# Optimization experiments

Measured on AMD Instinct MI355X. Metric: run time of the kernel, lower is better.

The kernel has to match this reference:

```python
import jax, jax.numpy as jnp
import numpy as np
from jax import lax

STRIDE = (1, 1)  # module init arg; stride slicing of the spectrum


def next_pow2(k: int) -> int:
    return 1 << (int(k) - 1).bit_length()


def setup_inputs() -> dict:
    key = jax.random.key(0)
    k1, k2, k3 = jax.random.split(key, 3)
    B, H, W, C, F = 16, 128, 128, 16, 32
    image = jax.random.normal(k1, (B, H, W, C), dtype=jnp.float32)
    # kernel shape per module: (2*H/stride_h, W/stride_w + 1, features, C)
    kh, kw = 2 * H // STRIDE[0], W // STRIDE[1] + 1
    kernel_real = jax.random.normal(k2, (kh, kw, F, C), dtype=jnp.float32)
    kernel_imag = jax.random.normal(k3, (kh, kw, F, C), dtype=jnp.float32)
    bias = jnp.zeros((F,), dtype=jnp.float32)
    return {"image": image, "kernel_real": kernel_real,
            "kernel_imag": kernel_imag, "bias": bias}


def reference(image, kernel_real, kernel_imag, bias):
    kernel = kernel_real + 1j * kernel_imag  # complex64 [kh, kw, F, C]
    B, H, W, C = image.shape
    padded = (2 * H - 1, 2 * W - 1)                       # "full" conv extent
    fast = (next_pow2(padded[0]), next_pow2(padded[1]))    # FFT-friendly pad
    fast_strided = (next_pow2(kernel.shape[0]), next_pow2(kernel.shape[1]))
    # rfft2 over spatial axes -> [B, fast_h, fast_w//2+1, C]
    F_img = jnp.fft.rfft2(image, s=fast, axes=(1, 2))
    F_img = F_img[:, ::STRIDE[0], ::STRIDE[1]]
    # channel contraction in Fourier space (vmap+sum in original == einsum)
    out_f = jnp.einsum('bhwc,hwfc->bhwf', F_img, kernel)
    # back to real space: [B, fast_strided_h, fast_strided_w, F]
    conv = jnp.fft.irfft2(out_f, s=fast_strided, axes=(1, 2))
    conv = conv + bias
    # crop to full-conv extent, then center-crop to "same" shape
    conv = conv[:, :padded[0], :padded[1], :]
    sh = (padded[0] - H) // 2
    sw = (padded[1] - W) // 2
    return lax.slice(conv, (0, sh, sw, 0),
                     (B, sh + H, sw + W, conv.shape[-1]))
```

## Files before the change

### kernel.cpp

```cpp
#include <hip/hip_runtime.h>
#include <math.h>


constexpr int Bn = 16, Cc = 16, Ff = 32, Hh = 128, Ww = 128, Nn = 256, WH = 129;

#define DEVINL __device__ __forceinline__
DEVINL float2 f2(float a, float b) { return make_float2(a, b); }
DEVINL float2 cmul(float2 a, float2 b) { return f2(a.x * b.x - a.y * b.y, a.x * b.y + a.y * b.x); }

DEVINL unsigned short f2bf(float f) { unsigned u = __float_as_uint(f); return (unsigned short)((u + 0x8000u) >> 16); }
DEVINL float bf2f(unsigned short h) { return __uint_as_float(((unsigned)h) << 16); }
DEVINL unsigned packbf(float a, float b) { return (unsigned)f2bf(a) | ((unsigned)f2bf(b) << 16); }
DEVINL ushort2 pk2(float2 z) { return make_ushort2(f2bf(z.x), f2bf(z.y)); }
DEVINL float2 up2(ushort2 u) { return f2(bf2f(u.x), bf2f(u.y)); }

typedef __attribute__((ext_vector_type(8))) short short8;
typedef __attribute__((ext_vector_type(4))) float f32x4;

DEVINL int IDX(int r, int e) { return r * 256 + ((e + r) & 255); }

template<int SGN>
DEVINL void fft16r(float2 v[16]) {
  float2 t;
#define SW(a,b) { t = v[a]; v[a] = v[b]; v[b] = t; }
  SW(1, 8) SW(2, 4) SW(3, 12) SW(5, 10) SW(7, 14) SW(11, 13)
#undef SW
  const float C1 = 0.92387953251128674f, C2 = 0.70710678118654752f, C3 = 0.38268343236508977f;
  const float Ct[8] = {1.f, C1, C2, C3, 0.f, -C3, -C2, -C1};
  const float St[8] = {0.f, C3, C2, C1, 1.f, C1, C2, C3};
#pragma unroll
  for (int len = 2; len <= 16; len <<= 1) {
    const int half = len >> 1, ts = 16 / len;
#pragma unroll
    for (int i = 0; i < 16; i += len) {
#pragma unroll
      for (int j = 0; j < half; ++j) {
        const float wr = Ct[j * ts];
        const float wi = (SGN > 0) ? St[j * ts] : -St[j * ts];
        float2 b = v[i + j + half];
        float2 tt = f2(wr * b.x - wi * b.y, wr * b.y + wi * b.x);
        float2 a = v[i + j];
        v[i + j]        = f2(a.x + tt.x, a.y + tt.y);
        v[i + j + half] = f2(a.x - tt.x, a.y - tt.y);
      }
    }
  }
}

template<int SGN>
DEVINL void twiddle16(float2 v[16], int t) {
  const float unit = (SGN > 0) ? 0.024543692606170259f : -0.024543692606170259f;
  float sb, cb;
  __sincosf(unit * (float)t, &sb, &cb);
  float2 W[16];
  W[1] = f2(cb, sb);
#pragma unroll
  for (int k = 2; k < 16; ++k) W[k] = cmul(W[k >> 1], W[k - (k >> 1)]);
#pragma unroll
  for (int k = 1; k < 16; ++k) v[k] = cmul(v[k], W[k]);
}

template<int SGN>
DEVINL void fft256_mid(float2 v[16], float2* __restrict__ lds, int r, int t) {
  fft16r<SGN>(v);
  twiddle16<SGN>(v, t);
#pragma unroll
  for (int k = 0; k < 16; ++k) lds[IDX(r, t * 16 + ((k + t) & 15))] = v[k];
#pragma unroll
  for (int n2 = 0; n2 < 16; ++n2) v[n2] = lds[IDX(r, n2 * 16 + ((t + n2) & 15))];
  fft16r<SGN>(v);
}

__global__ __launch_bounds__(256) void k1_rowfft(const float* __restrict__ img, ushort2* __restrict__ R) {
  __shared__ float2 lds[16 * 256];
  const int tid = threadIdx.x, r = tid >> 4, t = tid & 15;
  const int y = blockIdx.x, b = blockIdx.y;
  const float* ip = img + ((size_t)(b * Hh + y) * Ww) * Cc;
  for (int i = tid; i < Ww * Cc; i += 256) { int x = i >> 4, c = i & 15; lds[IDX(c, x)] = f2(ip[i], 0.f); }
  __syncthreads();
  float2 v[16];
#pragma unroll
  for (int j = 0; j < 8; ++j) v[j] = lds[IDX(r, t + 16 * j)];
#pragma unroll
  for (int j = 8; j < 16; ++j) v[j] = f2(0.f, 0.f);
  fft256_mid<-1>(v, lds, r, t);
#pragma unroll
  for (int k = 0; k < 8; ++k) lds[IDX(r, t + 16 * k)] = v[k];
  if (t == 0) lds[IDX(r, 128)] = v[8];
  __syncthreads();
  ushort2* rp = R + (size_t)b * WH * Hh * Cc + (size_t)y * Cc;
  for (int i = tid; i < WH * Cc; i += 256) {
    int w = i >> 4, c = i & 15;
    rp[(size_t)w * Hh * Cc + c] = pk2(lds[IDX(c, w)]);
  }
}

__global__ __launch_bounds__(256) void k2_colfft(const ushort2* __restrict__ R, ushort2* __restrict__ Fimg) {
  __shared__ float2 lds[16 * 256];
  const int tid = threadIdx.x, r = tid >> 4, t = tid & 15;
  const int w = blockIdx.x, b = blockIdx.y;
  const ushort2* rp = R + ((size_t)(b * WH + w) * Hh) * Cc;
  for (int i = tid; i < Hh * Cc; i += 256) { int y = i >> 4, c = i & 15; lds[IDX(c, y)] = up2(rp[i]); }
  __syncthreads();
  float2 v[16];
#pragma unroll
  for (int j = 0; j < 8; ++j) v[j] = lds[IDX(r, t + 16 * j)];
#pragma unroll
  for (int j = 8; j < 16; ++j) v[j] = f2(0.f, 0.f);
  fft256_mid<-1>(v, lds, r, t);
#pragma unroll
  for (int k2 = 0; k2 < 16; ++k2) lds[IDX(r, t + 16 * k2)] = v[k2];
  __syncthreads();
  ushort2* fp = Fimg + (size_t)w * 256 + b * 16;
  for (int i = tid; i < Nn * Cc; i += 256) {
    int h = i >> 4, c = i & 15;
    fp[(size_t)h * WH * 256 + c] = pk2(lds[IDX(c, h)]);
  }
}

constexpr int K3PTS = 8;
__global__ __launch_bounds__(256) void k3_mul(const ushort2* __restrict__ Fimg, const float* __restrict__ Kr,
                                              const float* __restrict__ Ki, ushort2* __restrict__ OF) {
  const int tid = threadIdx.x;
  const int wv = tid >> 6, ln = tid & 63;
  const int tile = wv & 1;
  const int w = blockIdx.x, h0 = blockIdx.y * 16 + (wv >> 1) * K3PTS;
  const int q = ln >> 4, fq = ln & 15, m0 = q & 1;
  const bool hi = (q >= 2);
  const int sh = hi ? 16 : 0;
  const unsigned negmask = hi ? 0x80008000u : 0u;

  uint4 a0[2], a1[2];
  float4 kr0[2], kr1[2], ki0[2], ki1[2];

  auto load = [&](int g, int p) {
    const size_t base = (size_t)(h0 + g) * WH + w;
    const uint4* ap = (const uint4*)(Fimg + base * 256);
    a0[p] = ap[fq * 4 + 2 * m0];
    a1[p] = ap[fq * 4 + 2 * m0 + 1];
    const float* krp = Kr + base * 512 + fq * 16 + tile * 256 + 8 * m0;
    const float* kip = Ki + base * 512 + fq * 16 + tile * 256 + 8 * m0;
    kr0[p] = *(const float4*)krp;  kr1[p] = *(const float4*)(krp + 4);
    ki0[p] = *(const float4*)kip;  ki1[p] = *(const float4*)(kip + 4);
  };
  auto compute = [&](int g, int p) {
    union U { unsigned u[4]; short8 s; };
    U ua;
    ua.u[0] = ((a0[p].x >> sh) & 0xffffu) | (((a0[p].y >> sh) & 0xffffu) << 16);
    ua.u[1] = ((a0[p].z >> sh) & 0xffffu) | (((a0[p].w >> sh) & 0xffffu) << 16);
    ua.u[2] = ((a1[p].x >> sh) & 0xffffu) | (((a1[p].y >> sh) & 0xffffu) << 16);
    ua.u[3] = ((a1[p].z >> sh) & 0xffffu) | (((a1[p].w >> sh) & 0xffffu) << 16);
    unsigned krP[4], kiP[4];
    krP[0] = packbf(kr0[p].x, kr0[p].y);  krP[1] = packbf(kr0[p].z, kr0[p].w);
    krP[2] = packbf(kr1[p].x, kr1[p].y);  krP[3] = packbf(kr1[p].z, kr1[p].w);
    kiP[0] = packbf(ki0[p].x, ki0[p].y);  kiP[1] = packbf(ki0[p].z, ki0[p].w);
    kiP[2] = packbf(ki1[p].x, ki1[p].y);  kiP[3] = packbf(ki1[p].z, ki1[p].w);
    U ubr, ubi;
#pragma unroll
    for (int j = 0; j < 4; ++j) {
      ubr.u[j] = (hi ? kiP[j] : krP[j]) ^ negmask;
      ubi.u[j] = hi ? krP[j] : kiP[j];
    }
    f32x4 accR = {0.f, 0.f, 0.f, 0.f}, accI = {0.f, 0.f, 0.f, 0.f};
    accR = __builtin_amdgcn_mfma_f32_16x16x32_bf16(ua.s, ubr.s, accR, 0, 0, 0);
    accI = __builtin_amdgcn_mfma_f32_16x16x32_bf16(ua.s, ubi.s, accI, 0, 0, 0);
    unsigned* op = (unsigned*)(OF + ((size_t)w * 256 + (h0 + g)) * 512);
#pragma unroll
    for (int reg = 0; reg < 4; ++reg)
      op[(4 * q + reg) * 32 + fq + 16 * tile] = packbf(accR[reg], accI[reg]);
  };

  load(0, 0);
#pragma unroll
  for (int g = 0; g < K3PTS; ++g) {
    if (g + 1 < K3PTS) load(g + 1, (g + 1) & 1);
    compute(g, g & 1);
  }
}

__global__ __launch_bounds__(512) void k4_colifft(const ushort2* __restrict__ OF, ushort2* __restrict__ T) {
  __shared__ float2 lds[32 * 256];
  const int tid = threadIdx.x, s = tid >> 4, t = tid & 15;
  const int bidx = blockIdx.x;
  const int b = bidx & 15, w = bidx >> 4;
  const int fh = tid & 15;
  const ushort4* ofp4 = (const ushort4*)OF + (size_t)w * 65536;
  for (int i = tid; i < Nn * 16; i += 512) {
    int h = i >> 4;
    ushort4 u = ofp4[(size_t)h * 256 + b * 16 + fh];
    lds[IDX(2 * fh, h)]     = f2(bf2f(u.x), bf2f(u.y));
    lds[IDX(2 * fh + 1, h)] = f2(bf2f(u.z), bf2f(u.w));
  }
  __syncthreads();
  float2 v[16];
#pragma unroll
  for (int j = 0; j < 16; ++j) v[j] = lds[IDX(s, t + 16 * j)];
  fft256_mid<1>(v, lds, s, t);
#pragma unroll
  for (int k2 = 3; k2 < 12; ++k2) lds[IDX(s, t + 16 * k2)] = v[k2];
  __syncthreads();
  ushort4* tp4 = (ushort4*)T + ((size_t)b * Hh * WH) * 16 + (size_t)w * 16;
  for (int i = tid; i < Hh * 16; i += 512) {
    int yp = i >> 4;
    float2 z0 = lds[IDX(2 * fh, 63 + yp)];
    float2 z1 = lds[IDX(2 * fh + 1, 63 + yp)];
    ushort4 st; st.x = f2bf(z0.x); st.y = f2bf(z0.y); st.z = f2bf(z1.x); st.w = f2bf(z1.y);
    tp4[(size_t)yp * WH * 16 + fh] = st;
  }
}

__global__ __launch_bounds__(512) void k5_rowifft(const ushort2* __restrict__ T, const float* __restrict__ bias,
                                                  float* __restrict__ out) {
  __shared__ float2 lds[32 * 256];
  const int tid = threadIdx.x, s = tid >> 4, t = tid & 15;
  const int yp = blockIdx.x, b = blockIdx.y;
  const int fh = tid & 15;
  const ushort4* tp4 = (const ushort4*)T + ((size_t)(b * Hh + yp) * WH) * 16;
  for (int i = tid; i < WH * 16; i += 512) {
    int w = i >> 4;
    ushort4 u = tp4[(size_t)w * 16 + fh];
    lds[IDX(2 * fh, w)]     = f2(bf2f(u.x), bf2f(u.y));
    lds[IDX(2 * fh + 1, w)] = f2(bf2f(u.z), bf2f(u.w));
  }
  __syncthreads();
  float2 v[16];
#pragma unroll
  for (int n1 = 0; n1 < 16; ++n1) {
    const int c = t + 16 * n1;
    if (c <= 128) v[n1] = lds[IDX(s, c)];
    else { float2 z = lds[IDX(s, 256 - c)]; v[n1] = f2(z.x, -z.y); }
  }
  fft256_mid<1>(v, lds, s, t);
#pragma unroll
  for (int k2 = 3; k2 < 12; ++k2) lds[IDX(s, t + 16 * k2)] = v[k2];
  __syncthreads();
  const float sc = 1.f / 65536.f;
  const float bv0 = bias[2 * fh], bv1 = bias[2 * fh + 1];
  float2* op = (float2*)(out + ((size_t)(b * Hh + yp) * Ww) * Ff);
  for (int i = tid; i < Ww * 16; i += 512) {
    int x = i >> 4;
    float re0 = lds[IDX(2 * fh, 63 + x)].x * sc + bv0;
    float re1 = lds[IDX(2 * fh + 1, 63 + x)].x * sc + bv1;
    op[(size_t)x * 16 + fh] = f2(re0, re1);
  }
}

extern "C" void kernel_launch(void* const* d_in, const int* in_sizes, int n_in,
                              void* d_out, int out_size, void* d_ws, size_t ws_size,
                              hipStream_t stream) {
  const float* img  = (const float*)d_in[0];
  const float* kr   = (const float*)d_in[1];
  const float* ki   = (const float*)d_in[2];
  const float* bias = (const float*)d_in[3];
  float* out = (float*)d_out;

  char* ws = (char*)d_ws;
  const size_t szF = (size_t)Nn * WH * Bn * Cc * sizeof(float2);
  ushort2* Fimg = (ushort2*)ws;
  ushort2* T    = (ushort2*)ws;
  ushort2* OF   = (ushort2*)(ws + szF);
  ushort2* R    = (ushort2*)(ws + szF);

  k1_rowfft <<<dim3(Hh, Bn),   256, 0, stream>>>(img, R);
  k2_colfft <<<dim3(WH, Bn),   256, 0, stream>>>(R, Fimg);
  k3_mul    <<<dim3(WH, 16),   256, 0, stream>>>(Fimg, kr, ki, OF);
  k4_colifft<<<dim3(WH * Bn),  512, 0, stream>>>(OF, T);
  k5_rowifft<<<dim3(Hh, Bn),   512, 0, stream>>>(T, bias, out);
}
```

Baseline: 150.2 us.

## Compute both feature tiles per wave in k3 and pack OF output as uint2

k3_mul now has each wave compute both 16-feature tiles for its frequency points, reusing the loaded image fragment across four MFMAs instead of splitting tiles across waves. Each wave handles 4 rows instead of 8, and the explicit double-buffered prefetch is dropped. The OF layout changes to interleave features f and f+16 in one uint2, and k4's unpacking is updated to match. The final output store becomes a nontemporal store. The aim is to halve the redundant image loads and widen stores, at the cost of relying on the compiler rather than explicit prefetch to hide load latency.

```diff
diff --git a/kernel.cpp b/kernel.cpp
--- a/kernel.cpp
+++ b/kernel.cpp
@@ -13,9 +13,11 @@
 DEVINL unsigned packbf(float a, float b) { return (unsigned)f2bf(a) | ((unsigned)f2bf(b) << 16); }
 DEVINL ushort2 pk2(float2 z) { return make_ushort2(f2bf(z.x), f2bf(z.y)); }
 DEVINL float2 up2(ushort2 u) { return f2(bf2f(u.x), bf2f(u.y)); }
+DEVINL float2 upu(unsigned u) { return f2(bf2f((unsigned short)(u & 0xffffu)), bf2f((unsigned short)(u >> 16))); }
 
 typedef __attribute__((ext_vector_type(8))) short short8;
 typedef __attribute__((ext_vector_type(4))) float f32x4;
+typedef __attribute__((ext_vector_type(2))) float fv2;
 
 DEVINL int IDX(int r, int e) { return r * 256 + ((e + r) & 255); }
 
@@ -118,63 +120,74 @@
   }
 }
 
-constexpr int K3PTS = 8;
+constexpr int K3PTS = 4;
 __global__ __launch_bounds__(256) void k3_mul(const ushort2* __restrict__ Fimg, const float* __restrict__ Kr,
                                               const float* __restrict__ Ki, ushort2* __restrict__ OF) {
   const int tid = threadIdx.x;
   const int wv = tid >> 6, ln = tid & 63;
-  const int tile = wv & 1;
-  const int w = blockIdx.x, h0 = blockIdx.y * 16 + (wv >> 1) * K3PTS;
+  const int w = blockIdx.x, h0 = blockIdx.y * 16 + wv * K3PTS;
   const int q = ln >> 4, fq = ln & 15, m0 = q & 1;
   const bool hi = (q >= 2);
   const int sh = hi ? 16 : 0;
   const unsigned negmask = hi ? 0x80008000u : 0u;
 
-  uint4 a0[2], a1[2];
-  float4 kr0[2], kr1[2], ki0[2], ki1[2];
-
-  auto load = [&](int g, int p) {
+  union U { unsigned u[4]; short8 s; };
+
+#pragma unroll
+  for (int g = 0; g < K3PTS; ++g) {
     const size_t base = (size_t)(h0 + g) * WH + w;
     const uint4* ap = (const uint4*)(Fimg + base * 256);
-    a0[p] = ap[fq * 4 + 2 * m0];
-    a1[p] = ap[fq * 4 + 2 * m0 + 1];
-    const float* krp = Kr + base * 512 + fq * 16 + tile * 256 + 8 * m0;
-    const float* kip = Ki + base * 512 + fq * 16 + tile * 256 + 8 * m0;
-    kr0[p] = *(const float4*)krp;  kr1[p] = *(const float4*)(krp + 4);
-    ki0[p] = *(const float4*)kip;  ki1[p] = *(const float4*)(kip + 4);
-  };
-  auto compute = [&](int g, int p) {
-    union U { unsigned u[4]; short8 s; };
+    const uint4 a0 = ap[fq * 4 + 2 * m0];
+    const uint4 a1 = ap[fq * 4 + 2 * m0 + 1];
+    const float* kb = Kr + base * 512 + fq * 16 + 8 * m0;
+    const float* ib = Ki + base * 512 + fq * 16 + 8 * m0;
+    const float4 kr00 = *(const float4*)kb;          const float4 kr01 = *(const float4*)(kb + 4);
+    const float4 kr10 = *(const float4*)(kb + 256);  const float4 kr11 = *(const float4*)(kb + 260);
+    const float4 ki00 = *(const float4*)ib;          const float4 ki01 = *(const float4*)(ib + 4);
+    const float4 ki10 = *(const float4*)(ib + 256);  const float4 ki11 = *(const float4*)(ib + 260);
+
     U ua;
-    ua.u[0] = ((a0[p].x >> sh) & 0xffffu) | (((a0[p].y >> sh) & 0xffffu) << 16);
-    ua.u[1] = ((a0[p].z >> sh) & 0xffffu) | (((a0[p].w >> sh) & 0xffffu) << 16);
-    ua.u[2] = ((a1[p].x >> sh) & 0xffffu) | (((a1[p].y >> sh) & 0xffffu) << 16);
-    ua.u[3] = ((a1[p].z >> sh) & 0xffffu) | (((a1[p].w >> sh) & 0xffffu) << 16);
-    unsigned krP[4], kiP[4];
-    krP[0] = packbf(kr0[p].x, kr0[p].y);  krP[1] = packbf(kr0[p].z, kr0[p].w);
-    krP[2] = packbf(kr1[p].x, kr1[p].y);  krP[3] = packbf(kr1[p].z, kr1[p].w);
-    kiP[0] = packbf(ki0[p].x, ki0[p].y);  kiP[1] = packbf(ki0[p].z, ki0[p].w);
-    kiP[2] = packbf(ki1[p].x, ki1[p].y);  kiP[3] = packbf(ki1[p].z, ki1[p].w);
-    U ubr, ubi;
-#pragma unroll
-    for (int j = 0; j < 4; ++j) {
-      ubr.u[j] = (hi ? kiP[j] : krP[j]) ^ negmask;
-      ubi.u[j] = hi ? krP[j] : kiP[j];
+    ua.u[0] = ((a0.x >> sh) & 0xffffu) | (((a0.y >> sh) & 0xffffu) << 16);
+    ua.u[1] = ((a0.z >> sh) & 0xffffu) | (((a0.w >> sh) & 0xffffu) << 16);
+    ua.u[2] = ((a1.x >> sh) & 0xffffu) | (((a1.y >> sh) & 0xffffu) << 16);
+    ua.u[3] = ((a1.z >> sh) & 0xffffu) | (((a1.w >> sh) & 0xffffu) << 16);
+
+    U ubr0, ubi0, ubr1, ubi1;
+    {
+      unsigned krP[4] = { packbf(kr00.x, kr00.y), packbf(kr00.z, kr00.w),
+                          packbf(kr01.x, kr01.y), packbf(kr01.z, kr01.w) };
+      unsigned kiP[4] = { packbf(ki00.x, ki00.y), packbf(ki00.z, ki00.w),
+                          packbf(ki01.x, ki01.y), packbf(ki01.z, ki01.w) };
+#pragma unroll
+      for (int j = 0; j < 4; ++j) {
+        ubr0.u[j] = (hi ? kiP[j] : krP[j]) ^ negmask;
+        ubi0.u[j] = hi ? krP[j] : kiP[j];
+      }
     }
-    f32x4 accR = {0.f, 0.f, 0.f, 0.f}, accI = {0.f, 0.f, 0.f, 0.f};
-    accR = __builtin_amdgcn_mfma_f32_16x16x32_bf16(ua.s, ubr.s, accR, 0, 0, 0);
-    accI = __builtin_amdgcn_mfma_f32_16x16x32_bf16(ua.s, ubi.s, accI, 0, 0, 0);
-    unsigned* op = (unsigned*)(OF + ((size_t)w * 256 + (h0 + g)) * 512);
+    {
+      unsigned krP[4] = { packbf(kr10.x, kr10.y), packbf(kr10.z, kr10.w),
+                          packbf(kr11.x, kr11.y), packbf(kr11.z, kr11.w) };
+      unsigned kiP[4] = { packbf(ki10.x, ki10.y), packbf(ki10.z, ki10.w),
+                          packbf(ki11.x, ki11.y), packbf(ki11.z, ki11.w) };
+#pragma unroll
+      for (int j = 0; j < 4; ++j) {
+        ubr1.u[j] = (hi ? kiP[j] : krP[j]) ^ negmask;
+        ubi1.u[j] = hi ? krP[j] : kiP[j];
+      }
+    }
+
+    f32x4 aR0 = {0.f, 0.f, 0.f, 0.f}, aI0 = {0.f, 0.f, 0.f, 0.f};
+    f32x4 aR1 = {0.f, 0.f, 0.f, 0.f}, aI1 = {0.f, 0.f, 0.f, 0.f};
+    aR0 = __builtin_amdgcn_mfma_f32_16x16x32_bf16(ua.s, ubr0.s, aR0, 0, 0, 0);
+    aI0 = __builtin_amdgcn_mfma_f32_16x16x32_bf16(ua.s, ubi0.s, aI0, 0, 0, 0);
+    aR1 = __builtin_amdgcn_mfma_f32_16x16x32_bf16(ua.s, ubr1.s, aR1, 0, 0, 0);
+    aI1 = __builtin_amdgcn_mfma_f32_16x16x32_bf16(ua.s, ubi1.s, aI1, 0, 0, 0);
+
+    uint2* op = (uint2*)(OF + ((size_t)w * 256 + (h0 + g)) * 512);
 #pragma unroll
     for (int reg = 0; reg < 4; ++reg)
-      op[(4 * q + reg) * 32 + fq + 16 * tile] = packbf(accR[reg], accI[reg]);
-  };
-
-  load(0, 0);
-#pragma unroll
-  for (int g = 0; g < K3PTS; ++g) {
-    if (g + 1 < K3PTS) load(g + 1, (g + 1) & 1);
-    compute(g, g & 1);
+      op[(4 * q + reg) * 16 + fq] = make_uint2(packbf(aR0[reg], aI0[reg]),
+                                               packbf(aR1[reg], aI1[reg]));
   }
 }
 
@@ -184,12 +197,12 @@
   const int bidx = blockIdx.x;
   const int b = bidx & 15, w = bidx >> 4;
   const int fh = tid & 15;
-  const ushort4* ofp4 = (const ushort4*)OF + (size_t)w * 65536;
+  const uint2* ofp2 = (const uint2*)OF + (size_t)w * 65536;
   for (int i = tid; i < Nn * 16; i += 512) {
     int h = i >> 4;
-    ushort4 u = ofp4[(size_t)h * 256 + b * 16 + fh];
-    lds[IDX(2 * fh, h)]     = f2(bf2f(u.x), bf2f(u.y));
-    lds[IDX(2 * fh + 1, h)] = f2(bf2f(u.z), bf2f(u.w));
+    uint2 u = ofp2[(size_t)h * 256 + b * 16 + fh];
+    lds[IDX(fh, h)]      = upu(u.x);
+    lds[IDX(fh + 16, h)] = upu(u.y);
   }
   __syncthreads();
   float2 v[16];
@@ -236,12 +249,13 @@
   __syncthreads();
   const float sc = 1.f / 65536.f;
   const float bv0 = bias[2 * fh], bv1 = bias[2 * fh + 1];
-  float2* op = (float2*)(out + ((size_t)(b * Hh + yp) * Ww) * Ff);
+  fv2* op = (fv2*)(out + ((size_t)(b * Hh + yp) * Ww) * Ff);
   for (int i = tid; i < Ww * 16; i += 512) {
     int x = i >> 4;
-    float re0 = lds[IDX(2 * fh, 63 + x)].x * sc + bv0;
-    float re1 = lds[IDX(2 * fh + 1, 63 + x)].x * sc + bv1;
-    op[(size_t)x * 16 + fh] = f2(re0, re1);
+    fv2 st;
+    st.x = lds[IDX(2 * fh, 63 + x)].x * sc + bv0;
+    st.y = lds[IDX(2 * fh + 1, 63 + x)].x * sc + bv1;
+    __builtin_nontemporal_store(st, &op[(size_t)x * 16 + fh]);
   }
 }
 
```

New measurement: 136.4 us. 9.2% less time.
